# Performance work log

Hardware: AMD Instinct MI355X
Metric: run time of the kernel (lower is better)

## Reference

```python
import jax, jax.numpy as jnp
import numpy as np

EMBED = 1024
HEADS = 16
DH = EMBED // HEADS
B, S = 2, 2048


def setup_inputs() -> dict:
    key = jax.random.key(0)
    ks = jax.random.split(key, 12)
    inp = {
        "k": jax.random.normal(ks[0], (B, S, EMBED), jnp.float32),
        "q": jax.random.normal(ks[1], (B, S, EMBED), jnp.float32),
        "v": jax.random.normal(ks[2], (B, S, EMBED), jnp.float32),
        "mask": jax.random.randint(ks[3], (B, 1, S, S), 0, 2, jnp.int32),
        # per-head projections (shared across heads, as in the torch module)
        "Wk": jax.random.normal(ks[4], (DH, DH), jnp.float32) / np.sqrt(DH),
        "bk": jnp.zeros((DH,), jnp.float32),
        "Wq": jax.random.normal(ks[5], (DH, DH), jnp.float32) / np.sqrt(DH),
        "bq": jnp.zeros((DH,), jnp.float32),
        "Wv": jax.random.normal(ks[6], (DH, DH), jnp.float32) / np.sqrt(DH),
        "bv": jnp.zeros((DH,), jnp.float32),
        "Wo": jax.random.normal(ks[7], (EMBED, EMBED), jnp.float32) / np.sqrt(EMBED),
        "bo": jnp.zeros((EMBED,), jnp.float32),
    }
    return inp


def reference(k, q, v, mask, Wk, bk, Wq, bq, Wv, bv, Wo, bo):
    b, s, _ = k.shape
    sq = q.shape[1]
    # [B,S,H,dh]
    kh = k.reshape(b, s, HEADS, DH)
    qh = q.reshape(b, sq, HEADS, DH)
    vh = v.reshape(b, s, HEADS, DH)
    # per-head linear (weight shared across heads): x @ W.T + b
    kh = kh @ Wk.T + bk
    qh = qh @ Wq.T + bq
    vh = vh @ Wv.T + bv
    # scores [B,H,Sq,Sk]
    product = jnp.einsum("bqhd,bkhd->bhqk", qh, kh)
    # masked_fill BEFORE scaling, as in the original
    product = jnp.where(mask == 0, jnp.float32(-1e20), product)
    product = product / np.sqrt(DH)
    scores = jax.nn.softmax(product, axis=-1)
    ctx = jnp.einsum("bhqk,bkhd->bqhd", scores, vh).reshape(b, sq, EMBED)
    return ctx @ Wo.T + bo
```

## Files before the change

kernel.cpp:

```cpp
#include <hip/hip_runtime.h>
#include <hip/hip_bf16.h>
#include <math.h>

#define EMBED 1024
#define HEADS 16
#define DH    64
#define BATCH 2
#define SEQ   2048

typedef __attribute__((ext_vector_type(8))) short bf16x8;
typedef __attribute__((ext_vector_type(4))) short bf16x4;
typedef __attribute__((ext_vector_type(4))) float f32x4;
typedef unsigned long long u64;

#define QSCALE 0.1803368801111244f

static __device__ __forceinline__ unsigned short f2bf(float x) {
    unsigned u = __builtin_bit_cast(unsigned, x);
    return (unsigned short)((u + 0x7fffu + ((u >> 16) & 1u)) >> 16);
}
static __device__ __forceinline__ unsigned pk2bf(float a, float b) {
    union { __hip_bfloat162 h2; unsigned u; } c;
    c.h2 = __float22bfloat162_rn(make_float2(a, b));
    return c.u;
}
static __device__ __forceinline__ void gl_lds16(const void* g, void* l) {
    __builtin_amdgcn_global_load_lds(
        (const __attribute__((address_space(1))) void*)g,
        (__attribute__((address_space(3))) void*)l, 16, 0, 0);
}

__global__ __launch_bounds__(256) void proj_mfma(
    const float* __restrict__ q, const float* __restrict__ k, const float* __restrict__ v,
    const float* __restrict__ Wq, const float* __restrict__ bq,
    const float* __restrict__ Wk, const float* __restrict__ bk,
    const float* __restrict__ Wv, const float* __restrict__ bv,
    unsigned short* __restrict__ qh, unsigned short* __restrict__ kh,
    unsigned short* __restrict__ vh)
{
    const int blk = blockIdx.x;
    const int which = blockIdx.y;
    const float* x; const float* W; const float* bias; unsigned short* out;
    if (which == 0)      { x = q; W = Wq; bias = bq; out = qh; }
    else if (which == 1) { x = k; W = Wk; bias = bk; out = kh; }
    else                 { x = v; W = Wv; bias = bv; out = vh; }
    const float oscale = (which == 0) ? QSCALE : 1.0f;

    __shared__ unsigned short Xs[64 * 72];
    __shared__ unsigned short Ws[64 * 72];

    const int t  = threadIdx.x;
    const int sr = t >> 2, sp = t & 3;

    {
        const float* xsrc = x + ((size_t)blk * 64 + sr) * 64 + sp * 16;
        unsigned o32[8];
#pragma unroll
        for (int u4 = 0; u4 < 4; ++u4) {
            float4 a = ((const float4*)xsrc)[u4];
            o32[u4 * 2 + 0] = pk2bf(a.x, a.y);
            o32[u4 * 2 + 1] = pk2bf(a.z, a.w);
        }
        *(uint4*)&Xs[sr * 72 + sp * 16]     = *(uint4*)&o32[0];
        *(uint4*)&Xs[sr * 72 + sp * 16 + 8] = *(uint4*)&o32[4];
        const float* wsrc = W + (size_t)sr * 64 + sp * 16;
#pragma unroll
        for (int u4 = 0; u4 < 4; ++u4) {
            float4 a = ((const float4*)wsrc)[u4];
            o32[u4 * 2 + 0] = pk2bf(a.x, a.y);
            o32[u4 * 2 + 1] = pk2bf(a.z, a.w);
        }
        *(uint4*)&Ws[sr * 72 + sp * 16]     = *(uint4*)&o32[0];
        *(uint4*)&Ws[sr * 72 + sp * 16 + 8] = *(uint4*)&o32[4];
    }
    __syncthreads();

    const int w    = t >> 6;
    const int lane = t & 63;
    const int l15  = lane & 15;
    const int quad = lane >> 4;

    bf16x8 af0 = *(const bf16x8*)&Xs[(w * 16 + l15) * 72 + quad * 8];
    bf16x8 af1 = *(const bf16x8*)&Xs[(w * 16 + l15) * 72 + 32 + quad * 8];

    f32x4 acc[4];
#pragma unroll
    for (int nt = 0; nt < 4; ++nt) {
        bf16x8 bf0 = *(const bf16x8*)&Ws[(nt * 16 + l15) * 72 + quad * 8];
        bf16x8 bf1 = *(const bf16x8*)&Ws[(nt * 16 + l15) * 72 + 32 + quad * 8];
        f32x4 a = {0, 0, 0, 0};
        a = __builtin_amdgcn_mfma_f32_16x16x32_bf16(af0, bf0, a, 0, 0, 0);
        a = __builtin_amdgcn_mfma_f32_16x16x32_bf16(af1, bf1, a, 0, 0, 0);
        acc[nt] = a;
    }

    const int bsidx = blk * 4 + w;
    const int b = bsidx >> 11, s = bsidx & 2047;
#pragma unroll
    for (int nt = 0; nt < 4; ++nt) {
        const int d = nt * 16 + l15;
        const float bb = bias[d];
#pragma unroll
        for (int r = 0; r < 4; ++r) {
            const int h = quad * 4 + r;
            out[(((size_t)b * HEADS + h) * SEQ + s) * DH + d] =
                f2bf((acc[nt][r] + bb) * oscale);
        }
    }
}

__global__ __launch_bounds__(256) void prep_kernel(
    const unsigned short* __restrict__ vh, unsigned short* __restrict__ vt,
    const int* __restrict__ mask, u64* __restrict__ bits,
    const float* __restrict__ Wo, unsigned short* __restrict__ Wob)
{
    __shared__ unsigned short Tt[64 * 72];
    const int bid = blockIdx.x;
    const int t   = threadIdx.x;

    if (bid < 1024) {
        const int st = bid & 31;
        const int bh = bid >> 5;
        const int r = t >> 2, p = t & 3;
        const unsigned short* src = vh + ((size_t)bh * SEQ + st * 64 + r) * DH + p * 16;
        *(uint4*)&Tt[r * 72 + p * 16]     = *(const uint4*)src;
        *(uint4*)&Tt[r * 72 + p * 16 + 8] = *(const uint4*)(src + 8);
        __syncthreads();
        union { unsigned short u[16]; uint4 v[2]; } o;
#pragma unroll
        for (int u = 0; u < 16; ++u) o.u[u] = Tt[(p * 16 + u) * 72 + r];
        unsigned short* dst = vt + ((size_t)bh * DH + r) * SEQ + st * 64 + p * 16;
        *(uint4*)dst       = o.v[0];
        *(uint4*)(dst + 8) = o.v[1];
    } else if (bid < 1536) {
        const int idx = (bid - 1024) * 256 + t;
        const int4* src = (const int4*)(mask + (size_t)idx * 64);
        u64 w = 0;
#pragma unroll
        for (int u = 0; u < 16; ++u) {
            int4 m = src[u];
            u64 nib = (m.x != 0 ? 1ull : 0) | (m.y != 0 ? 2ull : 0) |
                      (m.z != 0 ? 4ull : 0) | (m.w != 0 ? 8ull : 0);
            w |= nib << (u * 4);
        }
        bits[idx] = w;
    } else {
        const int i = ((bid - 1536) * 256 + t) * 8;
        float4 a = ((const float4*)(Wo + i))[0];
        float4 b = ((const float4*)(Wo + i))[1];
        unsigned o32[4] = {pk2bf(a.x, a.y), pk2bf(a.z, a.w),
                           pk2bf(b.x, b.y), pk2bf(b.z, b.w)};
        *(uint4*)(Wob + i) = *(uint4*)o32;
    }
}

__global__ __launch_bounds__(256, 4) void attn_kernel(
    const unsigned short* __restrict__ qh, const unsigned short* __restrict__ kh,
    const unsigned short* __restrict__ vt, const u64* __restrict__ mbits,
    unsigned short* __restrict__ ctx)
{
    const int bid = blockIdx.x;
    const int bh  = bid & 31;
    const int q0  = (bid >> 5) * 64;
    const int b   = bh >> 4;

    __shared__ unsigned char smem[32768];

    const int t    = threadIdx.x;
    const int hh   = t >> 7;
    const int w2   = (t >> 6) & 1;
    const int lane = t & 63;
    const int l15  = lane & 15;
    const int quad = lane >> 4;

    unsigned short* KtH = (unsigned short*)(smem + hh * 16384);
    unsigned short* VtH = KtH + 4096;

    const int srow   = lane >> 3;
    const int schunk = (lane & 7) ^ srow;

    bf16x8 qf[2][2];
#pragma unroll
    for (int g = 0; g < 2; ++g) {
        const unsigned short* qb =
            qh + ((size_t)bh * SEQ + q0 + w2 * 32 + g * 16 + l15) * DH + quad * 8;
        qf[g][0] = *(const bf16x8*)qb;
        qf[g][1] = *(const bf16x8*)(qb + 32);
    }

    f32x4 O[2][4];
#pragma unroll
    for (int g = 0; g < 2; ++g)
#pragma unroll
        for (int dt = 0; dt < 4; ++dt) O[g][dt] = f32x4{0, 0, 0, 0};
    f32x4 Osum[2] = {f32x4{0, 0, 0, 0}, f32x4{0, 0, 0, 0}};
    const bf16x4 ones = {(short)0x3F80, (short)0x3F80, (short)0x3F80, (short)0x3F80};

    const unsigned short* kbase = kh + (size_t)bh * SEQ * DH + (size_t)hh * 1024 * DH
                                  + (size_t)srow * DH + schunk * 8;
    const unsigned short* vbase = vt + (size_t)bh * DH * SEQ + hh * 1024
                                  + (size_t)srow * SEQ + schunk * 8;
    const u64* mrow0 = mbits + ((size_t)b * SEQ + q0 + w2 * 32 + l15) * (SEQ / 64) + hh * 16;
    const u64* mrow1 = mrow0 + 16 * (SEQ / 64);

    for (int kt = 0; kt < 16; ++kt) {
        __syncthreads();
        if (w2 == 0) {
            const unsigned short* g0 = kbase + (size_t)kt * 64 * DH;
#pragma unroll
            for (int i = 0; i < 8; ++i)
                gl_lds16(g0 + (size_t)i * 8 * DH, (unsigned char*)KtH + i * 1024);
        } else {
            const unsigned short* g0 = vbase + kt * 64;
#pragma unroll
            for (int i = 0; i < 8; ++i)
                gl_lds16(g0 + (size_t)i * 8 * SEQ, (unsigned char*)VtH + i * 1024);
        }
        const u64 mb0 = mrow0[kt];
        const u64 mb1 = mrow1[kt];
        __syncthreads();

        bf16x4 p[2][4];
        const int rx = l15 & 7;
#pragma unroll
        for (int st = 0; st < 4; ++st) {
            const int r = st * 16 + l15;
            bf16x8 kf0 = *(const bf16x8*)&KtH[r * 64 + ((quad ^ rx)) * 8];
            bf16x8 kf1 = *(const bf16x8*)&KtH[r * 64 + ((quad ^ rx) ^ 4) * 8];
#pragma unroll
            for (int g = 0; g < 2; ++g) {
                f32x4 sa = {0, 0, 0, 0};
                sa = __builtin_amdgcn_mfma_f32_16x16x32_bf16(kf0, qf[g][0], sa, 0, 0, 0);
                sa = __builtin_amdgcn_mfma_f32_16x16x32_bf16(kf1, qf[g][1], sa, 0, 0, 0);
                const unsigned nib = (unsigned)((g ? mb1 : mb0) >> (st * 16 + quad * 4)) & 0xFu;
                float p0 = (nib & 1u) ? exp2f(sa[0]) : 0.f;
                float p1 = (nib & 2u) ? exp2f(sa[1]) : 0.f;
                float p2 = (nib & 4u) ? exp2f(sa[2]) : 0.f;
                float p3 = (nib & 8u) ? exp2f(sa[3]) : 0.f;
                union { unsigned u2[2]; bf16x4 v; } pu;
                pu.u2[0] = pk2bf(p0, p1);
                pu.u2[1] = pk2bf(p2, p3);
                p[g][st] = pu.v;
                Osum[g] = __builtin_amdgcn_mfma_f32_16x16x16bf16_1k(p[g][st], ones, Osum[g], 0, 0, 0);
            }
        }

#pragma unroll
        for (int dt = 0; dt < 4; ++dt) {
            const int d = dt * 16 + l15;
            const int dx = l15 & 7;
#pragma unroll
            for (int st = 0; st < 4; ++st) {
                const int ch = (st * 2 + (quad >> 1)) ^ dx;
                bf16x4 vb = *(const bf16x4*)&VtH[d * 64 + ch * 8 + (quad & 1) * 4];
                O[0][dt] = __builtin_amdgcn_mfma_f32_16x16x16bf16_1k(p[0][st], vb, O[0][dt], 0, 0, 0);
                O[1][dt] = __builtin_amdgcn_mfma_f32_16x16x16bf16_1k(p[1][st], vb, O[1][dt], 0, 0, 0);
            }
        }
    }

    float* Obuf = (float*)smem;
    float* Ls   = ((float*)smem) + 64 * 68;

    __syncthreads();
    if (hh == 0) {
#pragma unroll
        for (int g = 0; g < 2; ++g) {
#pragma unroll
            for (int dt = 0; dt < 4; ++dt)
#pragma unroll
                for (int r = 0; r < 4; ++r)
                    Obuf[(w2 * 32 + g * 16 + quad * 4 + r) * 68 + dt * 16 + l15] = O[g][dt][r];
            if (l15 == 0) {
#pragma unroll
                for (int r = 0; r < 4; ++r)
                    Ls[w2 * 32 + g * 16 + quad * 4 + r] = Osum[g][r];
            }
        }
    }
    __syncthreads();
    if (hh == 1) {
#pragma unroll
        for (int g = 0; g < 2; ++g) {
            float invr[4];
#pragma unroll
            for (int r = 0; r < 4; ++r) {
                const int row = w2 * 32 + g * 16 + quad * 4 + r;
                invr[r] = 1.0f / (Osum[g][r] + Ls[row]);
            }
#pragma unroll
            for (int r = 0; r < 4; ++r) {
                const int row = w2 * 32 + g * 16 + quad * 4 + r;
                unsigned short* dst = ctx + ((size_t)bh * SEQ + q0 + row) * DH + l15;
#pragma unroll
                for (int dt = 0; dt < 4; ++dt) {
                    const float val = O[g][dt][r] + Obuf[row * 68 + dt * 16 + l15];
                    dst[dt * 16] = f2bf(val * invr[r]);
                }
            }
        }
    }
}

__global__ __launch_bounds__(256) void outproj_mfma(
    const unsigned short* __restrict__ ctx, const unsigned short* __restrict__ Wob,
    const float* __restrict__ bo, float* __restrict__ out)
{
    const int n0 = blockIdx.x * 64;
    const int m0 = blockIdx.y * 64;
    const int b  = m0 / SEQ;
    const int s0 = m0 % SEQ;

    __shared__ unsigned short At[64 * 72];
    __shared__ unsigned short Wt[64 * 72];

    const int t    = threadIdx.x;
    const int w    = t >> 6;
    const int lane = t & 63;
    const int l15  = lane & 15;
    const int quad = lane >> 4;
    const int sr = t >> 2, sp = t & 3;

    f32x4 acc[4] = {f32x4{0,0,0,0}, f32x4{0,0,0,0}, f32x4{0,0,0,0}, f32x4{0,0,0,0}};

    for (int kt = 0; kt < HEADS; ++kt) {
        __syncthreads();
        {
            const unsigned short* as =
                ctx + (((size_t)b * HEADS + kt) * SEQ + s0 + sr) * DH + sp * 16;
            *(uint4*)&At[sr * 72 + sp * 16]     = *(const uint4*)as;
            *(uint4*)&At[sr * 72 + sp * 16 + 8] = *(const uint4*)(as + 8);
            const unsigned short* wsrc =
                Wob + (size_t)(n0 + sr) * EMBED + kt * 64 + sp * 16;
            *(uint4*)&Wt[sr * 72 + sp * 16]     = *(const uint4*)wsrc;
            *(uint4*)&Wt[sr * 72 + sp * 16 + 8] = *(const uint4*)(wsrc + 8);
        }
        __syncthreads();

        bf16x8 bf0 = *(const bf16x8*)&Wt[(w * 16 + l15) * 72 + quad * 8];
        bf16x8 bf1 = *(const bf16x8*)&Wt[(w * 16 + l15) * 72 + 32 + quad * 8];
#pragma unroll
        for (int mt = 0; mt < 4; ++mt) {
            bf16x8 af0 = *(const bf16x8*)&At[(mt * 16 + l15) * 72 + quad * 8];
            bf16x8 af1 = *(const bf16x8*)&At[(mt * 16 + l15) * 72 + 32 + quad * 8];
            acc[mt] = __builtin_amdgcn_mfma_f32_16x16x32_bf16(af0, bf0, acc[mt], 0, 0, 0);
            acc[mt] = __builtin_amdgcn_mfma_f32_16x16x32_bf16(af1, bf1, acc[mt], 0, 0, 0);
        }
    }

    const float bv = bo[n0 + w * 16 + l15];
#pragma unroll
    for (int mt = 0; mt < 4; ++mt) {
#pragma unroll
        for (int r = 0; r < 4; ++r) {
            out[(size_t)(m0 + mt * 16 + quad * 4 + r) * EMBED + n0 + w * 16 + l15] =
                acc[mt][r] + bv;
        }
    }
}

extern "C" void kernel_launch(void* const* d_in, const int* in_sizes, int n_in,
                              void* d_out, int out_size, void* d_ws, size_t ws_size,
                              hipStream_t stream) {
    const float* k    = (const float*)d_in[0];
    const float* q    = (const float*)d_in[1];
    const float* v    = (const float*)d_in[2];
    const int*   mask = (const int*)  d_in[3];
    const float* Wk   = (const float*)d_in[4];
    const float* bk   = (const float*)d_in[5];
    const float* Wq   = (const float*)d_in[6];
    const float* bq   = (const float*)d_in[7];
    const float* Wv   = (const float*)d_in[8];
    const float* bv   = (const float*)d_in[9];
    const float* Wo   = (const float*)d_in[10];
    const float* bo   = (const float*)d_in[11];
    float* out = (float*)d_out;

    const size_t TEN = (size_t)BATCH * HEADS * SEQ * DH;
    unsigned short* qh_bf = (unsigned short*)d_ws;
    unsigned short* kh_bf = qh_bf + TEN;
    unsigned short* vh_bf = kh_bf + TEN;
    unsigned short* vt_bf = vh_bf + TEN;
    unsigned short* ctxb  = vt_bf + TEN;
    unsigned short* Wob   = ctxb + TEN;
    u64*            mbits = (u64*)(Wob + EMBED * EMBED);

    proj_mfma<<<dim3(BATCH * SEQ * HEADS / 64, 3), 256, 0, stream>>>(
        q, k, v, Wq, bq, Wk, bk, Wv, bv, qh_bf, kh_bf, vh_bf);
    prep_kernel<<<dim3(2048), 256, 0, stream>>>(
        vh_bf, vt_bf, mask, mbits, Wo, Wob);
    attn_kernel<<<dim3((SEQ / 64) * BATCH * HEADS), 256, 0, stream>>>(
        qh_bf, kh_bf, vt_bf, mbits, ctxb);
    outproj_mfma<<<dim3(EMBED / 64, BATCH * SEQ / 64), 256, 0, stream>>>(
        ctxb, Wob, bo, out);
}
```

Before: 249.5 us.

## Double-buffer K/V tiles in attention and operand tiles in out-projection

Both the attention kernel and the output-projection GEMM now prefetch the next tile into a second LDS buffer using direct global-to-LDS loads while computing on the current one. This removes one barrier per iteration and hides load latency. The out-projection also switches from padded register-staged tiles to XOR-swizzled direct LDS loads. Doubling attention LDS to 64KB lowers the occupancy bound from 4 to 2 blocks per CU, which may reduce latency hiding elsewhere.

```diff
diff --git a/kernel.cpp b/kernel.cpp
--- a/kernel.cpp
+++ b/kernel.cpp
@@ -154,7 +154,7 @@
     }
 }
 
-__global__ __launch_bounds__(256, 4) void attn_kernel(
+__global__ __launch_bounds__(256, 2) void attn_kernel(
     const unsigned short* __restrict__ qh, const unsigned short* __restrict__ kh,
     const unsigned short* __restrict__ vt, const u64* __restrict__ mbits,
     unsigned short* __restrict__ ctx)
@@ -164,7 +164,7 @@
     const int q0  = (bid >> 5) * 64;
     const int b   = bh >> 4;
 
-    __shared__ unsigned char smem[32768];
+    __shared__ unsigned char smem[65536];
 
     const int t    = threadIdx.x;
     const int hh   = t >> 7;
@@ -173,9 +173,6 @@
     const int l15  = lane & 15;
     const int quad = lane >> 4;
 
-    unsigned short* KtH = (unsigned short*)(smem + hh * 16384);
-    unsigned short* VtH = KtH + 4096;
-
     const int srow   = lane >> 3;
     const int schunk = (lane & 7) ^ srow;
 
@@ -203,22 +200,42 @@
     const u64* mrow0 = mbits + ((size_t)b * SEQ + q0 + w2 * 32 + l15) * (SEQ / 64) + hh * 16;
     const u64* mrow1 = mrow0 + 16 * (SEQ / 64);
 
+    if (w2 == 0) {
+        unsigned char* Kd = smem + hh * 16384;
+#pragma unroll
+        for (int i = 0; i < 8; ++i)
+            gl_lds16(kbase + (size_t)i * 8 * DH, Kd + i * 1024);
+    } else {
+        unsigned char* Vd = smem + hh * 16384 + 8192;
+#pragma unroll
+        for (int i = 0; i < 8; ++i)
+            gl_lds16(vbase + (size_t)i * 8 * SEQ, Vd + i * 1024);
+    }
+    u64 pm0 = mrow0[0], pm1 = mrow1[0];
+    __syncthreads();
+
     for (int kt = 0; kt < 16; ++kt) {
-        __syncthreads();
-        if (w2 == 0) {
-            const unsigned short* g0 = kbase + (size_t)kt * 64 * DH;
-#pragma unroll
-            for (int i = 0; i < 8; ++i)
-                gl_lds16(g0 + (size_t)i * 8 * DH, (unsigned char*)KtH + i * 1024);
-        } else {
-            const unsigned short* g0 = vbase + kt * 64;
-#pragma unroll
-            for (int i = 0; i < 8; ++i)
-                gl_lds16(g0 + (size_t)i * 8 * SEQ, (unsigned char*)VtH + i * 1024);
-        }
-        const u64 mb0 = mrow0[kt];
-        const u64 mb1 = mrow1[kt];
-        __syncthreads();
+        if (kt < 15) {
+            const int bn = (kt + 1) & 1;
+            if (w2 == 0) {
+                unsigned char* Kd = smem + bn * 32768 + hh * 16384;
+                const unsigned short* g0 = kbase + (size_t)(kt + 1) * 64 * DH;
+#pragma unroll
+                for (int i = 0; i < 8; ++i)
+                    gl_lds16(g0 + (size_t)i * 8 * DH, Kd + i * 1024);
+            } else {
+                unsigned char* Vd = smem + bn * 32768 + hh * 16384 + 8192;
+                const unsigned short* g0 = vbase + (kt + 1) * 64;
+#pragma unroll
+                for (int i = 0; i < 8; ++i)
+                    gl_lds16(g0 + (size_t)i * 8 * SEQ, Vd + i * 1024);
+            }
+        }
+        const u64 mb0 = pm0, mb1 = pm1;
+        if (kt < 15) { pm0 = mrow0[kt + 1]; pm1 = mrow1[kt + 1]; }
+
+        const unsigned short* KtH = (const unsigned short*)(smem + (kt & 1) * 32768 + hh * 16384);
+        const unsigned short* VtH = KtH + 4096;
 
         bf16x4 p[2][4];
         const int rx = l15 & 7;
@@ -257,12 +274,12 @@
                 O[1][dt] = __builtin_amdgcn_mfma_f32_16x16x16bf16_1k(p[1][st], vb, O[1][dt], 0, 0, 0);
             }
         }
+        __syncthreads();
     }
 
     float* Obuf = (float*)smem;
     float* Ls   = ((float*)smem) + 64 * 68;
 
-    __syncthreads();
     if (hh == 0) {
 #pragma unroll
         for (int g = 0; g < 2; ++g) {
@@ -302,7 +319,7 @@
     }
 }
 
-__global__ __launch_bounds__(256) void outproj_mfma(
+__global__ __launch_bounds__(256, 4) void outproj_mfma(
     const unsigned short* __restrict__ ctx, const unsigned short* __restrict__ Wob,
     const float* __restrict__ bo, float* __restrict__ out)
 {
@@ -311,41 +328,67 @@
     const int b  = m0 / SEQ;
     const int s0 = m0 % SEQ;
 
-    __shared__ unsigned short At[64 * 72];
-    __shared__ unsigned short Wt[64 * 72];
+    __shared__ unsigned char smem[32768];
 
     const int t    = threadIdx.x;
     const int w    = t >> 6;
     const int lane = t & 63;
     const int l15  = lane & 15;
     const int quad = lane >> 4;
-    const int sr = t >> 2, sp = t & 3;
+    const int srow   = lane >> 3;
+    const int schunk = (lane & 7) ^ srow;
+
+    const unsigned short* abase = ctx + ((size_t)b * HEADS * SEQ + s0 + srow) * DH + schunk * 8;
+    const unsigned short* wbase = Wob + (size_t)(n0 + srow) * EMBED + schunk * 8;
 
     f32x4 acc[4] = {f32x4{0,0,0,0}, f32x4{0,0,0,0}, f32x4{0,0,0,0}, f32x4{0,0,0,0}};
 
-    for (int kt = 0; kt < HEADS; ++kt) {
-        __syncthreads();
-        {
-            const unsigned short* as =
-                ctx + (((size_t)b * HEADS + kt) * SEQ + s0 + sr) * DH + sp * 16;
-            *(uint4*)&At[sr * 72 + sp * 16]     = *(const uint4*)as;
-            *(uint4*)&At[sr * 72 + sp * 16 + 8] = *(const uint4*)(as + 8);
-            const unsigned short* wsrc =
-                Wob + (size_t)(n0 + sr) * EMBED + kt * 64 + sp * 16;
-            *(uint4*)&Wt[sr * 72 + sp * 16]     = *(const uint4*)wsrc;
-            *(uint4*)&Wt[sr * 72 + sp * 16 + 8] = *(const uint4*)(wsrc + 8);
-        }
-        __syncthreads();
-
-        bf16x8 bf0 = *(const bf16x8*)&Wt[(w * 16 + l15) * 72 + quad * 8];
-        bf16x8 bf1 = *(const bf16x8*)&Wt[(w * 16 + l15) * 72 + 32 + quad * 8];
+    {
+        unsigned char* Ab = smem;
+        unsigned char* Wb = smem + 8192;
+#pragma unroll
+        for (int j = 0; j < 4; ++j) {
+            const int idx = w * 4 + j;
+            if (idx < 8)
+                gl_lds16(abase + (size_t)idx * 8 * DH, Ab + idx * 1024);
+            else
+                gl_lds16(wbase + (size_t)(idx - 8) * 8 * EMBED, Wb + (idx - 8) * 1024);
+        }
+    }
+    __syncthreads();
+
+    for (int kt = 0; kt < 16; ++kt) {
+        if (kt < 15) {
+            const int ktn = kt + 1;
+            unsigned char* Ab = smem + (ktn & 1) * 16384;
+            unsigned char* Wb = Ab + 8192;
+#pragma unroll
+            for (int j = 0; j < 4; ++j) {
+                const int idx = w * 4 + j;
+                if (idx < 8)
+                    gl_lds16(abase + (size_t)ktn * SEQ * DH + (size_t)idx * 8 * DH,
+                             Ab + idx * 1024);
+                else
+                    gl_lds16(wbase + (size_t)(idx - 8) * 8 * EMBED + ktn * 64,
+                             Wb + (idx - 8) * 1024);
+            }
+        }
+
+        const unsigned short* At = (const unsigned short*)(smem + (kt & 1) * 16384);
+        const unsigned short* Wt = At + 4096;
+        const int rx = l15 & 7;
+        const int c0 = ((quad ^ rx)) * 8;
+
+        bf16x8 bf0 = *(const bf16x8*)&Wt[(w * 16 + l15) * 64 + c0];
+        bf16x8 bf1 = *(const bf16x8*)&Wt[(w * 16 + l15) * 64 + (c0 ^ 32)];
 #pragma unroll
         for (int mt = 0; mt < 4; ++mt) {
-            bf16x8 af0 = *(const bf16x8*)&At[(mt * 16 + l15) * 72 + quad * 8];
-            bf16x8 af1 = *(const bf16x8*)&At[(mt * 16 + l15) * 72 + 32 + quad * 8];
+            bf16x8 af0 = *(const bf16x8*)&At[(mt * 16 + l15) * 64 + c0];
+            bf16x8 af1 = *(const bf16x8*)&At[(mt * 16 + l15) * 64 + (c0 ^ 32)];
             acc[mt] = __builtin_amdgcn_mfma_f32_16x16x32_bf16(af0, bf0, acc[mt], 0, 0, 0);
             acc[mt] = __builtin_amdgcn_mfma_f32_16x16x32_bf16(af1, bf1, acc[mt], 0, 0, 0);
         }
+        __syncthreads();
     }
 
     const float bv = bo[n0 + w * 16 + l15];
```

New measurement: 245.4 us. About the same (-1.6%).
